# Performance work log

Hardware: AMD Instinct MI355X
Metric: run time of the kernel (lower is better)

The kernel has to match this reference:

```python
import jax, jax.numpy as jnp
import numpy as np
from jax import lax

NEG = -1e30  # log-space 'zero' that stays finite for stable grads


def _logadd3(a, b, c):
    m = jnp.maximum(jnp.maximum(a, b), c)
    return m + jnp.log(jnp.exp(a - m) + jnp.exp(b - m) + jnp.exp(c - m))


def _logadd2(a, b):
    m = jnp.maximum(a, b)
    return m + jnp.log(jnp.exp(a - m) + jnp.exp(b - m))


def setup_inputs() -> dict:
    key = jax.random.key(0)
    k1, k2, k3 = jax.random.split(key, 3)
    B, T, V, L = 64, 2000, 512, 200
    logits = jax.random.normal(k1, (B, T, V), dtype=jnp.float32)
    # keep input lengths well above 2*L+1 so all paths are feasible
    input_lengths = (T - jax.random.randint(k2, (B,), 0, 256)).astype(jnp.int32)
    targets = jax.random.randint(k3, (B, L), 0, V, dtype=jnp.int32)  # 0 == pad == blank
    return {"logits": logits, "input_lengths": input_lengths, "targets": targets}


def ctc_loss_sum(logits, input_lengths, targets):
    B, T, V = logits.shape
    L = targets.shape[1]
    S = 2 * L + 1

    lp = jax.nn.log_softmax(logits, axis=-1)  # [B,T,V]

    # compact nonzero targets per row (masked_select equivalent, fixed shape)
    mask = targets != 0
    tlen = mask.sum(-1)  # [B] target_lengths
    pos = jnp.where(mask, jnp.cumsum(mask, axis=1) - 1, L)
    compact = jnp.zeros_like(targets).at[jnp.arange(B)[:, None], pos].set(targets, mode="drop")

    # extended label sequence: blank, y1, blank, y2, ..., blank  -> [B,S]
    s_idx = jnp.arange(S)
    lab_idx = jnp.clip((s_idx - 1) // 2, 0, L - 1)
    ext = jnp.where(s_idx % 2 == 1, compact[:, lab_idx], 0)  # [B,S]

    # skip transition s-2 -> s allowed iff label at s is non-blank and differs from s-2
    ext_m2 = jnp.pad(ext, ((0, 0), (2, 0)))[:, :S]
    skip_ok = (ext != 0) & (ext != ext_m2) & (s_idx >= 2)  # [B,S]

    lpT = jnp.transpose(lp, (1, 0, 2))  # [T,B,V], scan over time

    # init: alpha_0[0]=lp(blank), alpha_0[1]=lp(y1)
    lp0_ext = jnp.take_along_axis(lpT[0], ext[:, :2], axis=1)  # [B,2]
    alpha0 = jnp.full((B, S), NEG, dtype=lp.dtype).at[:, :2].set(lp0_ext)

    def step(alpha, inp):
        lp_t, t = inp
        a1 = jnp.pad(alpha, ((0, 0), (1, 0)), constant_values=NEG)[:, :S]
        a2 = jnp.pad(alpha, ((0, 0), (2, 0)), constant_values=NEG)[:, :S]
        a2 = jnp.where(skip_ok, a2, NEG)
        lp_e = jnp.take_along_axis(lp_t, ext, axis=1)  # [B,S]
        new = _logadd3(alpha, a1, a2) + lp_e
        active = (t < input_lengths)[:, None]
        return jnp.where(active, new, alpha), None

    alphaT, _ = lax.scan(step, alpha0, (lpT[1:], jnp.arange(1, T)))

    # read out at final blank (2*tlen) and final label (2*tlen-1)
    e1 = (2 * tlen)[:, None]
    e2 = (2 * tlen - 1)
    a1 = jnp.take_along_axis(alphaT, e1, axis=1)[:, 0]
    a2 = jnp.where(e2 >= 0,
                   jnp.take_along_axis(alphaT, jnp.clip(e2, 0)[:, None], axis=1)[:, 0],
                   NEG)
    ll = _logadd2(a1, a2)  # [B] log p(targets | logits)
    return -jnp.sum(ll)


def reference(logits, input_lengths, targets):
    return ctc_loss_sum(logits, input_lengths, targets)
```

## Files before the change

### kernel.cpp

```cpp
#include <hip/hip_runtime.h>

#define B_ 64
#define T_ 2000
#define V_ 512
#define L_ 200

typedef _Float16 half4 __attribute__((ext_vector_type(4)));

__device__ __forceinline__ float dpp_shr1_f(float x) {
  return __int_as_float(__builtin_amdgcn_update_dpp(0, __float_as_int(x), 0x138, 0xf, 0xf, true));
}
__device__ __forceinline__ int dpp_shr1_i(int x) {
  return __builtin_amdgcn_update_dpp(0, x, 0x138, 0xf, 0xf, true);
}
#define DPPADD(v, ctrl, rmask)                                                              \
  v += __int_as_float(__builtin_amdgcn_update_dpp(0, __float_as_int(v), ctrl, rmask, 0xf, true));


__global__ __launch_bounds__(64) void k0_compact(const int* __restrict__ targets,
                                                 int* __restrict__ compact,
                                                 int* __restrict__ tlen,
                                                 float* __restrict__ out) {
  const int b = blockIdx.x;
  const int lane = threadIdx.x;
  __shared__ int cbuf[256];
#pragma unroll
  for (int c = 0; c < 4; ++c) cbuf[c * 64 + lane] = 0;
  __syncthreads();
  int base = 0;
#pragma unroll
  for (int c = 0; c < 4; ++c) {
    const int l = c * 64 + lane;
    const int v = (l < L_) ? targets[b * L_ + l] : 0;
    const unsigned long long mk = __ballot(v != 0);
    const int pos = base + __popcll(mk & ((1ull << lane) - 1ull));
    if (v != 0) cbuf[pos] = v;
    base += __popcll(mk);
  }
  __syncthreads();
#pragma unroll
  for (int c = 0; c < 4; ++c) compact[b * 256 + c * 64 + lane] = cbuf[c * 64 + lane];
  if (lane == 0) {
    tlen[b] = base;
    if (b == 0) out[0] = 0.0f;
  }
}

__global__ __launch_bounds__(256) void k1_probs(float* __restrict__ logits,
                                                const int* __restrict__ compact,
                                                float* __restrict__ blank) {
  const int wave = threadIdx.x >> 6;
  const int lane = threadIdx.x & 63;
  const int r0 = (blockIdx.x * 4 + wave) * 2;
  const int b = r0 / T_;
  float* rp0 = logits + (size_t)r0 * V_;
  float* rp1 = rp0 + V_;
  const float4 xa0 = *(const float4*)(rp0 + 4 * lane);
  const float4 xa1 = *(const float4*)(rp0 + 256 + 4 * lane);
  const float4 xb0 = *(const float4*)(rp1 + 4 * lane);
  const float4 xb1 = *(const float4*)(rp1 + 256 + 4 * lane);
  const float ea0 = __expf(xa0.x), ea1 = __expf(xa0.y), ea2 = __expf(xa0.z), ea3 = __expf(xa0.w);
  const float ea4 = __expf(xa1.x), ea5 = __expf(xa1.y), ea6 = __expf(xa1.z), ea7 = __expf(xa1.w);
  const float eb0 = __expf(xb0.x), eb1 = __expf(xb0.y), eb2 = __expf(xb0.z), eb3 = __expf(xb0.w);
  const float eb4 = __expf(xb1.x), eb5 = __expf(xb1.y), eb6 = __expf(xb1.z), eb7 = __expf(xb1.w);
  float ra = ((ea0 + ea1) + (ea2 + ea3)) + ((ea4 + ea5) + (ea6 + ea7));
  float rb = ((eb0 + eb1) + (eb2 + eb3)) + ((eb4 + eb5) + (eb6 + eb7));
  DPPADD(ra, 0x111, 0xf); DPPADD(rb, 0x111, 0xf);
  DPPADD(ra, 0x112, 0xf); DPPADD(rb, 0x112, 0xf);
  DPPADD(ra, 0x114, 0xf); DPPADD(rb, 0x114, 0xf);
  DPPADD(ra, 0x118, 0xf); DPPADD(rb, 0x118, 0xf);
  DPPADD(ra, 0x142, 0xa); DPPADD(rb, 0x142, 0xa);
  DPPADD(ra, 0x143, 0xc); DPPADD(rb, 0x143, 0xc);
  const float suma = __int_as_float(__builtin_amdgcn_readlane(__float_as_int(ra), 63));
  const float sumb = __int_as_float(__builtin_amdgcn_readlane(__float_as_int(rb), 63));
  const float inva = 32.0f / suma;
  const float invb = 32.0f / sumb;
  __shared__ float prob[4][2][512];
  *(float4*)(&prob[wave][0][4 * lane]) = make_float4(ea0, ea1, ea2, ea3);
  *(float4*)(&prob[wave][0][256 + 4 * lane]) = make_float4(ea4, ea5, ea6, ea7);
  *(float4*)(&prob[wave][1][4 * lane]) = make_float4(eb0, eb1, eb2, eb3);
  *(float4*)(&prob[wave][1][256 + 4 * lane]) = make_float4(eb4, eb5, eb6, eb7);
  __syncthreads();
  const int4 c4 = *(const int4*)(compact + b * 256 + 4 * lane);
  const int l0 = 4 * lane;
  const bool v0 = l0 + 0 < L_, v1 = l0 + 1 < L_, v2 = l0 + 2 < L_, v3 = l0 + 3 < L_;
  half4 ha, hb;
  ha.x = (_Float16)(v0 ? prob[wave][0][c4.x] * inva : 0.0f);
  ha.y = (_Float16)(v1 ? prob[wave][0][c4.y] * inva : 0.0f);
  ha.z = (_Float16)(v2 ? prob[wave][0][c4.z] * inva : 0.0f);
  ha.w = (_Float16)(v3 ? prob[wave][0][c4.w] * inva : 0.0f);
  hb.x = (_Float16)(v0 ? prob[wave][1][c4.x] * invb : 0.0f);
  hb.y = (_Float16)(v1 ? prob[wave][1][c4.y] * invb : 0.0f);
  hb.z = (_Float16)(v2 ? prob[wave][1][c4.z] * invb : 0.0f);
  hb.w = (_Float16)(v3 ? prob[wave][1][c4.w] * invb : 0.0f);
  *(half4*)((char*)rp0 + 8 * lane) = ha;
  *(half4*)((char*)rp1 + 8 * lane) = hb;
  if (lane == 0) {
    const int t0 = r0 - b * T_;
    *(float2*)(blank + (b << 11) + t0) = make_float2(ea0 * inva, eb0 * invb);
  }
}

__global__ __launch_bounds__(64, 1) void k2_alpha(const float* __restrict__ pe,
                                                  const int* __restrict__ lens,
                                                  const int* __restrict__ compact,
                                                  const int* __restrict__ tlenp,
                                                  const float* __restrict__ blank,
                                                  float* __restrict__ out) {
  const int b = blockIdx.x;
  const int lane = threadIdx.x;
  const char* lbase = (const char*)(pe + (size_t)b * (T_ * V_)) + 8 * lane;
  const float* bl = blank + (b << 11);
  const int len = lens[b];

  const int4 c4 = *(const int4*)(compact + b * 256 + 4 * lane);
  const int cm1 = __shfl_up(c4.w, 1);
  const float m0 = (lane > 0 && c4.x != 0 && c4.x != cm1) ? 1.0f : 0.0f;
  const float m1 = (c4.y != 0 && c4.y != c4.x) ? 1.0f : 0.0f;
  const float m2 = (c4.z != 0 && c4.z != c4.y) ? 1.0f : 0.0f;
  const float m3 = (c4.w != 0 && c4.w != c4.z) ? 1.0f : 0.0f;

  float a0 = 0.f, a1 = 0.f, a2 = 0.f, a3 = 0.f, a4 = 0.f, a5 = 0.f, a6 = 0.f, a7 = 0.f;
  {
    const half4 h0 = *(const half4*)(lbase);
    const float pb0 = bl[0];
    if (lane == 0) { a0 = pb0; a1 = (float)h0.x; }
  }
  int E = 0;
  float fac = 1.0f;

  half4 LB0[8], LB1[8], LB2[8], LB3[8];
  float4 BLa0, BLa1, BLa2, BLa3, BLb0, BLb1, BLb2, BLb3;

#define LOADC(S, CIDX)                                                       \
  {                                                                          \
    int c8_ = (CIDX) * 8;                                                    \
    if (c8_ > T_ - 8) c8_ = T_ - 8;                                          \
    const char* rp_ = lbase + (size_t)c8_ * (V_ * 4);                        \
    _Pragma("unroll") for (int u = 0; u < 8; ++u)                            \
        LB##S[u] = *(const half4*)(rp_ + u * (V_ * 4));                      \
    BLa##S = *(const float4*)(bl + c8_);                                     \
    BLb##S = *(const float4*)(bl + c8_ + 4);                                 \
  }

#define STEP8(S, CIDX, ULO, MASKED)                                          \
  {                                                                          \
    const int tf_ = (CIDX) * 8;                                              \
    const float blv_[8] = {BLa##S.x, BLa##S.y, BLa##S.z, BLa##S.w,           \
                           BLb##S.x, BLb##S.y, BLb##S.z, BLb##S.w};          \
    _Pragma("unroll") for (int u = 0; u < 8; ++u) {                          \
      if (u >= (ULO)) {                                                      \
        const half4 hq = LB##S[u];                                           \
        const float qx = (float)hq.x, qy = (float)hq.y;                      \
        const float qz = (float)hq.z, qw = (float)hq.w;                      \
        const float pbv = blv_[u];                                           \
        const float s1 = dpp_shr1_f(a7) * fac;               \
        float n0 = (a0 + s1) * pbv;                                          \
        float n1 = fmaf(m0, s1, a0 + a1) * qx;                               \
        float n2 = (a2 + a1) * pbv;                                          \
        float n3 = fmaf(m1, a1, a2 + a3) * qy;                               \
        float n4 = (a4 + a3) * pbv;                                          \
        float n5 = fmaf(m2, a3, a4 + a5) * qz;                               \
        float n6 = (a6 + a5) * pbv;                                          \
        float n7 = fmaf(m3, a5, a6 + a7) * qw;                               \
        if (MASKED) {                                                        \
          const bool act = (tf_ + u) < len;                                  \
          n0 = act ? n0 : a0; n1 = act ? n1 : a1;                            \
          n2 = act ? n2 : a2; n3 = act ? n3 : a3;                            \
          n4 = act ? n4 : a4; n5 = act ? n5 : a5;                            \
          n6 = act ? n6 : a6; n7 = act ? n7 : a7;                            \
        }                                                                    \
        a0 = n0; a1 = n1; a2 = n2; a3 = n3;                                  \
        a4 = n4; a5 = n5; a6 = n6; a7 = n7;                                  \
      }                                                                      \
    }                                                                        \
  }

#define RENORM                                                               \
  {                                                                          \
    const float mx = fmaxf(fmaxf(fmaxf(a0, a1), fmaxf(a2, a3)),              \
                           fmaxf(fmaxf(a4, a5), fmaxf(a6, a7)));             \
    const bool dead = (mx == 0.0f);                                          \
    int e_ = (int)((__float_as_uint(mx) >> 23) & 0xff) - 127;                \
    if (dead) e_ = 0;                                                        \
    const float sc_ = __int_as_float((unsigned)(127 - e_) << 23);            \
    a0 *= sc_; a1 *= sc_; a2 *= sc_; a3 *= sc_;                              \
    a4 *= sc_; a5 *= sc_; a6 *= sc_; a7 *= sc_;                              \
    const int En_ = E + e_;                                                  \
    const int EnP_ = dpp_shr1_i(En_);                                        \
    E = dead ? EnP_ : En_;                                                   \
    const int Ep_ = dpp_shr1_i(E);                                           \
    const int d_ = Ep_ - E;                                                  \
    int dc_ = d_ < -126 ? -126 : (d_ > 126 ? 126 : d_);                      \
    fac = (d_ < -126) ? 0.0f : __int_as_float((unsigned)(dc_ + 127) << 23);  \
  }

  LOADC(0, 0); LOADC(1, 1); LOADC(2, 2); LOADC(3, 3);
  const int nfull = len >> 3;
  const int rem = len & 7;

  STEP8(0, 0, 1, 0);
  LOADC(0, 4);
  RENORM;

  int c = 1;
  while (c + 4 <= nfull) {
    STEP8(1, c, 0, 0);     LOADC(1, c + 4); RENORM;
    STEP8(2, c + 1, 0, 0); LOADC(2, c + 5); RENORM;
    STEP8(3, c + 2, 0, 0); LOADC(3, c + 6); RENORM;
    STEP8(0, c + 3, 0, 0); LOADC(0, c + 7); RENORM;
    c += 4;
  }
  while (c < nfull) {
    switch (c & 3) {
      case 0: STEP8(0, c, 0, 0); break;
      case 1: STEP8(1, c, 0, 0); break;
      case 2: STEP8(2, c, 0, 0); break;
      default: STEP8(3, c, 0, 0); break;
    }
    RENORM;
    c++;
  }
  if (rem) {
    switch (c & 3) {
      case 0: STEP8(0, c, 0, 1); break;
      case 1: STEP8(1, c, 0, 1); break;
      case 2: STEP8(2, c, 0, 1); break;
      default: STEP8(3, c, 0, 1); break;
    }
  }
#undef LOADC
#undef STEP8
#undef RENORM

  __shared__ float sval[512];
  __shared__ int sE[64];
  sval[lane * 8 + 0] = a0; sval[lane * 8 + 1] = a1;
  sval[lane * 8 + 2] = a2; sval[lane * 8 + 3] = a3;
  sval[lane * 8 + 4] = a4; sval[lane * 8 + 5] = a5;
  sval[lane * 8 + 6] = a6; sval[lane * 8 + 7] = a7;
  sE[lane] = E;
  __syncthreads();
  if (lane == 0) {
    const int tl = tlenp[b];
    const int e1 = 2 * tl;
    const int e2 = e1 - 1;
    const float v1 = sval[e1];
    const int E1 = sE[e1 >> 3];
    const float v2 = (e2 >= 0) ? sval[e2] : 0.0f;
    const int E2 = (e2 >= 0) ? sE[e2 >> 3] : E1;
    const int Em = (E1 > E2) ? E1 : E2;
    const float v = ldexpf(v1, E1 - Em) + ldexpf(v2, E2 - Em);
    const float ll = __logf(v) + (float)Em * 0.69314718056f - (float)len * 3.46573590280f;
    atomicAdd(out, -ll);
  }
}

extern "C" void kernel_launch(void* const* d_in, const int* in_sizes, int n_in,
                              void* d_out, int out_size, void* d_ws, size_t ws_size,
                              hipStream_t stream) {
  float* logits = (float*)d_in[0];
  const int* input_lengths = (const int*)d_in[1];
  const int* targets = (const int*)d_in[2];
  float* out = (float*)d_out;
  int* compact = (int*)d_ws;
  int* tlen = compact + B_ * 256;
  float* blank = (float*)((char*)d_ws + 131072);

  k0_compact<<<B_, 64, 0, stream>>>(targets, compact, tlen, out);
  k1_probs<<<(B_ * T_) / 8, 256, 0, stream>>>(logits, compact, blank);
  k2_alpha<<<B_, 64, 0, stream>>>(logits, input_lengths, compact, tlen, blank, out);
}
```

Before: 494.9 us.

## Fuse softmax gather and alpha recursion into one producer-consumer kernel per batch

Replaces the three-kernel pipeline with a single 512-thread block per batch row. Seven producer waves compute per-row softmax normalizers and gather target probabilities for 8-timestep chunks into a double-buffered shared-memory ring, while one consumer wave runs the scaled alpha recursion from that ring. This removes the global fp16 write-back and re-read of the gathered probabilities and the separate launches. In exchange only 64 blocks run, so the full logits read must be carried by 64 CUs, and each round ends in a block-wide barrier that couples producer and consumer pace.

```diff
diff --git a/kernel.cpp b/kernel.cpp
--- a/kernel.cpp
+++ b/kernel.cpp
@@ -4,6 +4,8 @@
 #define T_ 2000
 #define V_ 512
 #define L_ 200
+#define CPR 7
+
 
 typedef _Float16 half4 __attribute__((ext_vector_type(4)));
 
@@ -16,163 +18,141 @@
 #define DPPADD(v, ctrl, rmask)                                                              \
   v += __int_as_float(__builtin_amdgcn_update_dpp(0, __float_as_int(v), ctrl, rmask, 0xf, true));
 
-
-__global__ __launch_bounds__(64) void k0_compact(const int* __restrict__ targets,
-                                                 int* __restrict__ compact,
-                                                 int* __restrict__ tlen,
-                                                 float* __restrict__ out) {
+__global__ void kz(float* __restrict__ out) { out[0] = 0.0f; }
+
+__global__ __launch_bounds__(512, 1) void ctc_fused(const float* __restrict__ logits,
+                                                    const int* __restrict__ lens,
+                                                    const int* __restrict__ targets,
+                                                    float* __restrict__ out) {
   const int b = blockIdx.x;
-  const int lane = threadIdx.x;
-  __shared__ int cbuf[256];
-#pragma unroll
-  for (int c = 0; c < 4; ++c) cbuf[c * 64 + lane] = 0;
+  const int wid = threadIdx.x >> 6;
+  const int lane = threadIdx.x & 63;
+
+  __shared__ __align__(16) _Float16 ring[2][CPR][8][256];
+  __shared__ __align__(16) float ringbl[2][CPR][8];
+  __shared__ int cmp[256];
+  __shared__ int tl_s;
+  __shared__ float sval[512];
+  __shared__ int sE[64];
+
+  if (wid == 0) {
+    cmp[lane] = 0; cmp[64 + lane] = 0; cmp[128 + lane] = 0; cmp[192 + lane] = 0;
+    int base = 0;
+#pragma unroll
+    for (int cc = 0; cc < 4; ++cc) {
+      const int l = cc * 64 + lane;
+      const int v = (l < L_) ? targets[b * L_ + l] : 0;
+      const unsigned long long mk = __ballot(v != 0);
+      const int pos = base + __popcll(mk & ((1ull << lane) - 1ull));
+      if (v != 0) cmp[pos] = v;
+      base += __popcll(mk);
+    }
+    if (lane == 0) tl_s = base;
+  }
   __syncthreads();
-  int base = 0;
-#pragma unroll
-  for (int c = 0; c < 4; ++c) {
-    const int l = c * 64 + lane;
-    const int v = (l < L_) ? targets[b * L_ + l] : 0;
-    const unsigned long long mk = __ballot(v != 0);
-    const int pos = base + __popcll(mk & ((1ull << lane) - 1ull));
-    if (v != 0) cbuf[pos] = v;
-    base += __popcll(mk);
-  }
-  __syncthreads();
-#pragma unroll
-  for (int c = 0; c < 4; ++c) compact[b * 256 + c * 64 + lane] = cbuf[c * 64 + lane];
-  if (lane == 0) {
-    tlen[b] = base;
-    if (b == 0) out[0] = 0.0f;
-  }
-}
-
-__global__ __launch_bounds__(256) void k1_probs(float* __restrict__ logits,
-                                                const int* __restrict__ compact,
-                                                float* __restrict__ blank) {
-  const int wave = threadIdx.x >> 6;
-  const int lane = threadIdx.x & 63;
-  const int r0 = (blockIdx.x * 4 + wave) * 2;
-  const int b = r0 / T_;
-  float* rp0 = logits + (size_t)r0 * V_;
-  float* rp1 = rp0 + V_;
-  const float4 xa0 = *(const float4*)(rp0 + 4 * lane);
-  const float4 xa1 = *(const float4*)(rp0 + 256 + 4 * lane);
-  const float4 xb0 = *(const float4*)(rp1 + 4 * lane);
-  const float4 xb1 = *(const float4*)(rp1 + 256 + 4 * lane);
-  const float ea0 = __expf(xa0.x), ea1 = __expf(xa0.y), ea2 = __expf(xa0.z), ea3 = __expf(xa0.w);
-  const float ea4 = __expf(xa1.x), ea5 = __expf(xa1.y), ea6 = __expf(xa1.z), ea7 = __expf(xa1.w);
-  const float eb0 = __expf(xb0.x), eb1 = __expf(xb0.y), eb2 = __expf(xb0.z), eb3 = __expf(xb0.w);
-  const float eb4 = __expf(xb1.x), eb5 = __expf(xb1.y), eb6 = __expf(xb1.z), eb7 = __expf(xb1.w);
-  float ra = ((ea0 + ea1) + (ea2 + ea3)) + ((ea4 + ea5) + (ea6 + ea7));
-  float rb = ((eb0 + eb1) + (eb2 + eb3)) + ((eb4 + eb5) + (eb6 + eb7));
-  DPPADD(ra, 0x111, 0xf); DPPADD(rb, 0x111, 0xf);
-  DPPADD(ra, 0x112, 0xf); DPPADD(rb, 0x112, 0xf);
-  DPPADD(ra, 0x114, 0xf); DPPADD(rb, 0x114, 0xf);
-  DPPADD(ra, 0x118, 0xf); DPPADD(rb, 0x118, 0xf);
-  DPPADD(ra, 0x142, 0xa); DPPADD(rb, 0x142, 0xa);
-  DPPADD(ra, 0x143, 0xc); DPPADD(rb, 0x143, 0xc);
-  const float suma = __int_as_float(__builtin_amdgcn_readlane(__float_as_int(ra), 63));
-  const float sumb = __int_as_float(__builtin_amdgcn_readlane(__float_as_int(rb), 63));
-  const float inva = 32.0f / suma;
-  const float invb = 32.0f / sumb;
-  __shared__ float prob[4][2][512];
-  *(float4*)(&prob[wave][0][4 * lane]) = make_float4(ea0, ea1, ea2, ea3);
-  *(float4*)(&prob[wave][0][256 + 4 * lane]) = make_float4(ea4, ea5, ea6, ea7);
-  *(float4*)(&prob[wave][1][4 * lane]) = make_float4(eb0, eb1, eb2, eb3);
-  *(float4*)(&prob[wave][1][256 + 4 * lane]) = make_float4(eb4, eb5, eb6, eb7);
-  __syncthreads();
-  const int4 c4 = *(const int4*)(compact + b * 256 + 4 * lane);
+
+  const int len = lens[b];
+  const int nfull = len >> 3;
+  const int rem = len & 7;
+  const int nch = nfull + (rem ? 1 : 0);
+  const int R = (nch + CPR - 1) / CPR;
+  const int4 c4 = *(const int4*)(&cmp[4 * lane]);
+
   const int l0 = 4 * lane;
   const bool v0 = l0 + 0 < L_, v1 = l0 + 1 < L_, v2 = l0 + 2 < L_, v3 = l0 + 3 < L_;
-  half4 ha, hb;
-  ha.x = (_Float16)(v0 ? prob[wave][0][c4.x] * inva : 0.0f);
-  ha.y = (_Float16)(v1 ? prob[wave][0][c4.y] * inva : 0.0f);
-  ha.z = (_Float16)(v2 ? prob[wave][0][c4.z] * inva : 0.0f);
-  ha.w = (_Float16)(v3 ? prob[wave][0][c4.w] * inva : 0.0f);
-  hb.x = (_Float16)(v0 ? prob[wave][1][c4.x] * invb : 0.0f);
-  hb.y = (_Float16)(v1 ? prob[wave][1][c4.y] * invb : 0.0f);
-  hb.z = (_Float16)(v2 ? prob[wave][1][c4.z] * invb : 0.0f);
-  hb.w = (_Float16)(v3 ? prob[wave][1][c4.w] * invb : 0.0f);
-  *(half4*)((char*)rp0 + 8 * lane) = ha;
-  *(half4*)((char*)rp1 + 8 * lane) = hb;
-  if (lane == 0) {
-    const int t0 = r0 - b * T_;
-    *(float2*)(blank + (b << 11) + t0) = make_float2(ea0 * inva, eb0 * invb);
-  }
-}
-
-__global__ __launch_bounds__(64, 1) void k2_alpha(const float* __restrict__ pe,
-                                                  const int* __restrict__ lens,
-                                                  const int* __restrict__ compact,
-                                                  const int* __restrict__ tlenp,
-                                                  const float* __restrict__ blank,
-                                                  float* __restrict__ out) {
-  const int b = blockIdx.x;
-  const int lane = threadIdx.x;
-  const char* lbase = (const char*)(pe + (size_t)b * (T_ * V_)) + 8 * lane;
-  const float* bl = blank + (b << 11);
-  const int len = lens[b];
-
-  const int4 c4 = *(const int4*)(compact + b * 256 + 4 * lane);
-  const int cm1 = __shfl_up(c4.w, 1);
-  const float m0 = (lane > 0 && c4.x != 0 && c4.x != cm1) ? 1.0f : 0.0f;
-  const float m1 = (c4.y != 0 && c4.y != c4.x) ? 1.0f : 0.0f;
-  const float m2 = (c4.z != 0 && c4.z != c4.y) ? 1.0f : 0.0f;
-  const float m3 = (c4.w != 0 && c4.w != c4.z) ? 1.0f : 0.0f;
 
   float a0 = 0.f, a1 = 0.f, a2 = 0.f, a3 = 0.f, a4 = 0.f, a5 = 0.f, a6 = 0.f, a7 = 0.f;
-  {
-    const half4 h0 = *(const half4*)(lbase);
-    const float pb0 = bl[0];
-    if (lane == 0) { a0 = pb0; a1 = (float)h0.x; }
-  }
   int E = 0;
   float fac = 1.0f;
-
-  half4 LB0[8], LB1[8], LB2[8], LB3[8];
-  float4 BLa0, BLa1, BLa2, BLa3, BLb0, BLb1, BLb2, BLb3;
-
-#define LOADC(S, CIDX)                                                       \
+  float m0 = 0.f, m1 = 0.f, m2 = 0.f, m3 = 0.f;
+  half4 LB0[8], LB1[8];
+  float4 BLa0, BLb0, BLa1, BLb1;
+
+  if (wid == CPR) {
+    const int cm1 = __shfl_up(c4.w, 1);
+    m0 = (lane > 0 && c4.x != 0 && c4.x != cm1) ? 1.0f : 0.0f;
+    m1 = (c4.y != 0 && c4.y != c4.x) ? 1.0f : 0.0f;
+    m2 = (c4.z != 0 && c4.z != c4.y) ? 1.0f : 0.0f;
+    m3 = (c4.w != 0 && c4.w != c4.z) ? 1.0f : 0.0f;
+    if (lane == 0) a0 = 1.0f;
+  }
+
+  auto produce = [&](int rp) {
+    const int c = rp * CPR + wid;
+    if (c >= nch) return;
+    const int buf = rp & 1;
+    const float* rowp = logits + (size_t)b * (T_ * V_) + (size_t)c * (8 * V_);
+    float4 X[16];
+    float G[32];
+#pragma unroll
+    for (int r = 0; r < 8; ++r) {
+      X[2 * r] = *(const float4*)(rowp + r * V_ + 4 * lane);
+      X[2 * r + 1] = *(const float4*)(rowp + r * V_ + 256 + 4 * lane);
+    }
+#pragma unroll
+    for (int r = 0; r < 8; ++r) {
+      G[4 * r + 0] = rowp[r * V_ + c4.x];
+      G[4 * r + 1] = rowp[r * V_ + c4.y];
+      G[4 * r + 2] = rowp[r * V_ + c4.z];
+      G[4 * r + 3] = rowp[r * V_ + c4.w];
+    }
+#pragma unroll
+    for (int r = 0; r < 8; ++r) {
+      const float4 xe = X[2 * r], xo = X[2 * r + 1];
+      const float e0 = __expf(xe.x);
+      float s = ((e0 + __expf(xe.y)) + (__expf(xe.z) + __expf(xe.w))) +
+                ((__expf(xo.x) + __expf(xo.y)) + (__expf(xo.z) + __expf(xo.w)));
+      DPPADD(s, 0x111, 0xf); DPPADD(s, 0x112, 0xf); DPPADD(s, 0x114, 0xf);
+      DPPADD(s, 0x118, 0xf); DPPADD(s, 0x142, 0xa); DPPADD(s, 0x143, 0xc);
+      const float sum = __int_as_float(__builtin_amdgcn_readlane(__float_as_int(s), 63));
+      const float inv = 32.0f / sum;
+      half4 h;
+      h.x = (_Float16)(v0 ? __expf(G[4 * r + 0]) * inv : 0.0f);
+      h.y = (_Float16)(v1 ? __expf(G[4 * r + 1]) * inv : 0.0f);
+      h.z = (_Float16)(v2 ? __expf(G[4 * r + 2]) * inv : 0.0f);
+      h.w = (_Float16)(v3 ? __expf(G[4 * r + 3]) * inv : 0.0f);
+      *(half4*)(&ring[buf][wid][r][4 * lane]) = h;
+      if (lane == 0) ringbl[buf][wid][r] = e0 * inv;
+    }
+  };
+
+#define LDCHUNK(S, BUF, K)                                                   \
   {                                                                          \
-    int c8_ = (CIDX) * 8;                                                    \
-    if (c8_ > T_ - 8) c8_ = T_ - 8;                                          \
-    const char* rp_ = lbase + (size_t)c8_ * (V_ * 4);                        \
+    const int bf_ = (BUF), kk_ = (K);                                        \
     _Pragma("unroll") for (int u = 0; u < 8; ++u)                            \
-        LB##S[u] = *(const half4*)(rp_ + u * (V_ * 4));                      \
-    BLa##S = *(const float4*)(bl + c8_);                                     \
-    BLb##S = *(const float4*)(bl + c8_ + 4);                                 \
-  }
-
-#define STEP8(S, CIDX, ULO, MASKED)                                          \
+        LB##S[u] = *(const half4*)(&ring[bf_][kk_][u][4 * lane]);            \
+    BLa##S = *(const float4*)(&ringbl[bf_][kk_][0]);                         \
+    BLb##S = *(const float4*)(&ringbl[bf_][kk_][4]);                         \
+  }
+
+#define STEP8(S, CIDX, MASKED)                                               \
   {                                                                          \
     const int tf_ = (CIDX) * 8;                                              \
     const float blv_[8] = {BLa##S.x, BLa##S.y, BLa##S.z, BLa##S.w,           \
                            BLb##S.x, BLb##S.y, BLb##S.z, BLb##S.w};          \
     _Pragma("unroll") for (int u = 0; u < 8; ++u) {                          \
-      if (u >= (ULO)) {                                                      \
-        const half4 hq = LB##S[u];                                           \
-        const float qx = (float)hq.x, qy = (float)hq.y;                      \
-        const float qz = (float)hq.z, qw = (float)hq.w;                      \
-        const float pbv = blv_[u];                                           \
-        const float s1 = dpp_shr1_f(a7) * fac;               \
-        float n0 = (a0 + s1) * pbv;                                          \
-        float n1 = fmaf(m0, s1, a0 + a1) * qx;                               \
-        float n2 = (a2 + a1) * pbv;                                          \
-        float n3 = fmaf(m1, a1, a2 + a3) * qy;                               \
-        float n4 = (a4 + a3) * pbv;                                          \
-        float n5 = fmaf(m2, a3, a4 + a5) * qz;                               \
-        float n6 = (a6 + a5) * pbv;                                          \
-        float n7 = fmaf(m3, a5, a6 + a7) * qw;                               \
-        if (MASKED) {                                                        \
-          const bool act = (tf_ + u) < len;                                  \
-          n0 = act ? n0 : a0; n1 = act ? n1 : a1;                            \
-          n2 = act ? n2 : a2; n3 = act ? n3 : a3;                            \
-          n4 = act ? n4 : a4; n5 = act ? n5 : a5;                            \
-          n6 = act ? n6 : a6; n7 = act ? n7 : a7;                            \
-        }                                                                    \
-        a0 = n0; a1 = n1; a2 = n2; a3 = n3;                                  \
-        a4 = n4; a5 = n5; a6 = n6; a7 = n7;                                  \
+      const half4 hq = LB##S[u];                                             \
+      const float qx = (float)hq.x, qy = (float)hq.y;                        \
+      const float qz = (float)hq.z, qw = (float)hq.w;                        \
+      const float pbv = blv_[u];                                             \
+      const float s1 = dpp_shr1_f(a7) * fac;                 \
+      float n0 = (a0 + s1) * pbv;                                            \
+      float n1 = fmaf(m0, s1, a0 + a1) * qx;                                 \
+      float n2 = (a2 + a1) * pbv;                                            \
+      float n3 = fmaf(m1, a1, a2 + a3) * qy;                                 \
+      float n4 = (a4 + a3) * pbv;                                            \
+      float n5 = fmaf(m2, a3, a4 + a5) * qz;                                 \
+      float n6 = (a6 + a5) * pbv;                                            \
+      float n7 = fmaf(m3, a5, a6 + a7) * qw;                                 \
+      if (MASKED) {                                                          \
+        const bool act = (tf_ + u) < len;                                    \
+        n0 = act ? n0 : a0; n1 = act ? n1 : a1;                              \
+        n2 = act ? n2 : a2; n3 = act ? n3 : a3;                              \
+        n4 = act ? n4 : a4; n5 = act ? n5 : a5;                              \
+        n6 = act ? n6 : a6; n7 = act ? n7 : a7;                              \
       }                                                                      \
+      a0 = n0; a1 = n1; a2 = n2; a3 = n3;                                    \
+      a4 = n4; a5 = n5; a6 = n6; a7 = n7;                                    \
     }                                                                        \
   }
 
@@ -195,79 +175,75 @@
     fac = (d_ < -126) ? 0.0f : __int_as_float((unsigned)(dc_ + 127) << 23);  \
   }
 
-  LOADC(0, 0); LOADC(1, 1); LOADC(2, 2); LOADC(3, 3);
-  const int nfull = len >> 3;
-  const int rem = len & 7;
-
-  STEP8(0, 0, 1, 0);
-  LOADC(0, 4);
-  RENORM;
-
-  int c = 1;
-  while (c + 4 <= nfull) {
-    STEP8(1, c, 0, 0);     LOADC(1, c + 4); RENORM;
-    STEP8(2, c + 1, 0, 0); LOADC(2, c + 5); RENORM;
-    STEP8(3, c + 2, 0, 0); LOADC(3, c + 6); RENORM;
-    STEP8(0, c + 3, 0, 0); LOADC(0, c + 7); RENORM;
-    c += 4;
-  }
-  while (c < nfull) {
-    switch (c & 3) {
-      case 0: STEP8(0, c, 0, 0); break;
-      case 1: STEP8(1, c, 0, 0); break;
-      case 2: STEP8(2, c, 0, 0); break;
-      default: STEP8(3, c, 0, 0); break;
-    }
-    RENORM;
-    c++;
-  }
-  if (rem) {
-    switch (c & 3) {
-      case 0: STEP8(0, c, 0, 1); break;
-      case 1: STEP8(1, c, 0, 1); break;
-      case 2: STEP8(2, c, 0, 1); break;
-      default: STEP8(3, c, 0, 1); break;
-    }
-  }
-#undef LOADC
+  if (wid < CPR) produce(0);
+  __syncthreads();
+
+  for (int r = 0; r < R; ++r) {
+    if (wid < CPR) {
+      if (r + 1 < R) produce(r + 1);
+    } else {
+      const int c0 = r * CPR;
+      int kn = nfull - c0;
+      if (kn > CPR) kn = CPR;
+      if (kn > 0) {
+        LDCHUNK(0, r & 1, 0);
+        for (int k = 0; k < kn; ++k) {
+          if (k & 1) {
+            if (k + 1 < kn) LDCHUNK(0, r & 1, k + 1);
+            STEP8(1, 0, 0);
+          } else {
+            if (k + 1 < kn) LDCHUNK(1, r & 1, k + 1);
+            STEP8(0, 0, 0);
+          }
+          RENORM;
+        }
+      }
+    }
+    __syncthreads();
+  }
+
+  if (wid == CPR) {
+    if (rem) {
+      const int cM = nfull;
+      const int rM = cM / CPR;
+      const int kM = cM - rM * CPR;
+      LDCHUNK(0, rM & 1, kM);
+      STEP8(0, cM, 1);
+    }
+    sval[lane * 8 + 0] = a0; sval[lane * 8 + 1] = a1;
+    sval[lane * 8 + 2] = a2; sval[lane * 8 + 3] = a3;
+    sval[lane * 8 + 4] = a4; sval[lane * 8 + 5] = a5;
+    sval[lane * 8 + 6] = a6; sval[lane * 8 + 7] = a7;
+    sE[lane] = E;
+    asm volatile("s_waitcnt lgkmcnt(0)" ::: "memory");
+    if (lane == 0) {
+      const int tl = tl_s;
+      const int e1 = 2 * tl;
+      const int e2 = e1 - 1;
+      const float v1r = sval[e1];
+      const int E1 = sE[e1 >> 3];
+      const float v2r = (e2 >= 0) ? sval[e2] : 0.0f;
+      const int E2 = (e2 >= 0) ? sE[e2 >> 3] : E1;
+      const int Em = (E1 > E2) ? E1 : E2;
+      const float v = ldexpf(v1r, E1 - Em) + ldexpf(v2r, E2 - Em);
+      const float ll = __logf(v) + (float)Em * 0.69314718056f - (float)len * 3.46573590280f;
+      atomicAdd(out, -ll);
+    }
+  }
+#undef LDCHUNK
 #undef STEP8
 #undef RENORM
-
-  __shared__ float sval[512];
-  __shared__ int sE[64];
-  sval[lane * 8 + 0] = a0; sval[lane * 8 + 1] = a1;
-  sval[lane * 8 + 2] = a2; sval[lane * 8 + 3] = a3;
-  sval[lane * 8 + 4] = a4; sval[lane * 8 + 5] = a5;
-  sval[lane * 8 + 6] = a6; sval[lane * 8 + 7] = a7;
-  sE[lane] = E;
-  __syncthreads();
-  if (lane == 0) {
-    const int tl = tlenp[b];
-    const int e1 = 2 * tl;
-    const int e2 = e1 - 1;
-    const float v1 = sval[e1];
-    const int E1 = sE[e1 >> 3];
-    const float v2 = (e2 >= 0) ? sval[e2] : 0.0f;
-    const int E2 = (e2 >= 0) ? sE[e2 >> 3] : E1;
-    const int Em = (E1 > E2) ? E1 : E2;
-    const float v = ldexpf(v1, E1 - Em) + ldexpf(v2, E2 - Em);
-    const float ll = __logf(v) + (float)Em * 0.69314718056f - (float)len * 3.46573590280f;
-    atomicAdd(out, -ll);
-  }
 }
 
 extern "C" void kernel_launch(void* const* d_in, const int* in_sizes, int n_in,
                               void* d_out, int out_size, void* d_ws, size_t ws_size,
                               hipStream_t stream) {
-  float* logits = (float*)d_in[0];
+  const float* logits = (const float*)d_in[0];
   const int* input_lengths = (const int*)d_in[1];
   const int* targets = (const int*)d_in[2];
   float* out = (float*)d_out;
-  int* compact = (int*)d_ws;
-  int* tlen = compact + B_ * 256;
-  float* blank = (float*)((char*)d_ws + 131072);
-
-  k0_compact<<<B_, 64, 0, stream>>>(targets, compact, tlen, out);
-  k1_probs<<<(B_ * T_) / 8, 256, 0, stream>>>(logits, compact, blank);
-  k2_alpha<<<B_, 64, 0, stream>>>(logits, input_lengths, compact, tlen, blank, out);
-}
+  (void)d_ws; (void)ws_size; (void)in_sizes; (void)n_in; (void)out_size;
+
+  kz<<<1, 1, 0, stream>>>(out);
+  ctc_fused<<<B_, 512, 0, stream>>>(logits, input_lengths, targets, out);
+}
```

After: 523.1 us. 5.7% more time.
